# Kernel tuning notes

Hardware: AMD Instinct MI355X
Metric: run time of the kernel (lower is better)

## Reference

```python
import jax, jax.numpy as jnp
import numpy as np

BH, W, C, NHEAD = 512, 256, 128, 4
HEAD_DIM = C // NHEAD
EPS = 1e-5


def _xavier(key, shape):
    fan_out, fan_in = shape
    lim = np.sqrt(6.0 / (fan_in + fan_out)).astype(np.float32)
    return jax.random.uniform(key, shape, jnp.float32, -lim, lim)


def setup_inputs() -> dict:
    key = jax.random.key(0)
    ks = jax.random.split(key, 4)
    return {
        "feat_left": jax.random.normal(ks[0], (BH, W, C), jnp.float32),
        "feat_right": jax.random.normal(ks[1], (BH, W, C), jnp.float32),
        "l_proj_weight": _xavier(ks[2], (2 * C, C)),
        "r_proj_weight": _xavier(ks[3], (2 * C, C)),
        "l_proj_bias": jnp.zeros((2 * C,), jnp.float32),
        "r_proj_bias": jnp.zeros((2 * C,), jnp.float32),
        "l_out_weight": _xavier(jax.random.fold_in(key, 10), (C, C)),
        "l_out_bias": jnp.zeros((C,), jnp.float32),
        "r_out_weight": _xavier(jax.random.fold_in(key, 11), (C, C)),
        "r_out_bias": jnp.zeros((C,), jnp.float32),
        "norm_weight": jnp.ones((C,), jnp.float32),
        "norm_bias": jnp.zeros((C,), jnp.float32),
    }


def _layernorm(x, w, b):
    mu = jnp.mean(x, axis=-1, keepdims=True)
    var = jnp.mean(jnp.square(x - mu), axis=-1, keepdims=True)
    return (x - mu) * jax.lax.rsqrt(var + EPS) * w + b


def reference(feat_left, feat_right, l_proj_weight, r_proj_weight,
              l_proj_bias, r_proj_bias, l_out_weight, l_out_bias,
              r_out_weight, r_out_bias, norm_weight, norm_bias):
    bh, w, c = feat_left.shape
    e, hd = NHEAD, HEAD_DIM

    l_n = _layernorm(feat_left, norm_weight, norm_bias)
    r_n = _layernorm(feat_right, norm_weight, norm_bias)

    l_kv = l_n @ l_proj_weight.T + l_proj_bias
    r_kv = r_n @ r_proj_weight.T + r_proj_bias
    l_k, l_v = jnp.split(l_kv, 2, axis=-1)
    r_k, r_v = jnp.split(r_kv, 2, axis=-1)

    l_k = l_k.reshape(bh, w, e, hd)
    r_k = r_k.reshape(bh, w, e, hd)
    l_v = l_v.reshape(bh, w, e, hd)
    r_v = r_v.reshape(bh, w, e, hd)

    # shared score matrix [bh, heads, w_left, w_right]
    attn = jnp.einsum('nwec,nvec->newv', l_k, r_k) * 0.1

    # left attends over right positions (softmax over last axis)
    sm_l = jax.nn.softmax(attn, axis=-1)
    out_l = jnp.einsum('newv,nvec->nwec', sm_l, r_v).reshape(bh, w, c)

    # right attends over left positions (softmax over w axis of same scores)
    sm_r = jax.nn.softmax(attn, axis=2)
    out_r = jnp.einsum('newv,nwec->nvec', sm_r, l_v).reshape(bh, w, c)

    out_l = out_l @ l_out_weight.T + l_out_bias
    out_r = out_r @ r_out_weight.T + r_out_bias

    return feat_left + out_l, feat_right + out_r
```

## Files before the change

kernel.cpp:

```cpp
#include <hip/hip_runtime.h>
#include <hip/hip_bf16.h>

#define BH   512
#define NW   256
#define CC   128
#define TOK  (BH * NW)

typedef __attribute__((ext_vector_type(8))) short short8;
typedef __attribute__((ext_vector_type(4))) float f32x4;
typedef __attribute__((ext_vector_type(4))) int   i32x4;
typedef __attribute__((ext_vector_type(4))) unsigned short us4;
typedef __attribute__((ext_vector_type(2))) unsigned int u32x2;
typedef unsigned short ushort_t;

static __device__ __forceinline__ f32x4 mfma16(short8 a, short8 b, f32x4 c) {
    return __builtin_amdgcn_mfma_f32_16x16x32_bf16(a, b, c, 0, 0, 0);
}

static __device__ __forceinline__ unsigned int pk2(float a, float b) {
    __hip_bfloat162 h = __float22bfloat162_rn(make_float2(a, b));
    return *reinterpret_cast<unsigned int*>(&h);
}
static __device__ __forceinline__ ushort_t f2bf(float f) {
    unsigned int u = __float_as_uint(f);
    u = (u + 0x7fffu + ((u >> 16) & 1u)) >> 16;
    return (ushort_t)u;
}

__global__ __launch_bounds__(256)
void k_prep(const float* __restrict__ WpL, const float* __restrict__ WpR,
            const float* __restrict__ bpL, const float* __restrict__ bpR,
            const float* __restrict__ nw,  const float* __restrict__ nb,
            ushort_t* __restrict__ Wb, float* __restrict__ bias2)
{
    const int gid = blockIdx.x * 256 + threadIdx.x;
    const int row = gid >> 2;
    const int q   = gid & 3;
    const int side = row >> 8;
    const int o    = row & 255;
    const float* Wp = side ? WpR : WpL;
    const float* bp = side ? bpR : bpL;
    const float* wr = Wp + (size_t)o * 128 + q * 32;

    float acc = 0.f;
#pragma unroll
    for (int g = 0; g < 4; ++g) {
        const int c = q * 32 + g * 8;
        float4 wa = *(const float4*)(wr + g * 8);
        float4 wb = *(const float4*)(wr + g * 8 + 4);
        float4 ga = *(const float4*)(nw + c);
        float4 gb = *(const float4*)(nw + c + 4);
        float4 ba = *(const float4*)(nb + c);
        float4 bb = *(const float4*)(nb + c + 4);
        acc += wa.x*ba.x + wa.y*ba.y + wa.z*ba.z + wa.w*ba.w
             + wb.x*bb.x + wb.y*bb.y + wb.z*bb.z + wb.w*bb.w;
        u32x2 o0, o1;
        o0[0] = pk2(wa.x*ga.x, wa.y*ga.y);
        o0[1] = pk2(wa.z*ga.z, wa.w*ga.w);
        o1[0] = pk2(wb.x*gb.x, wb.y*gb.y);
        o1[1] = pk2(wb.z*gb.z, wb.w*gb.w);
        *(u32x2*)(Wb + (size_t)row * 128 + c)     = o0;
        *(u32x2*)(Wb + (size_t)row * 128 + c + 4) = o1;
    }
    acc += __shfl_xor(acc, 1);
    acc += __shfl_xor(acc, 2);
    if (q == 0) bias2[row] = bp[o] + acc;
}

__global__ __launch_bounds__(256)
void k_ln_proj(const float* __restrict__ featL, const float* __restrict__ featR,
               const ushort_t* __restrict__ Wb, const float* __restrict__ bias2,
               ushort_t* __restrict__ kvL,      ushort_t* __restrict__ kvR)
{
    const int side = blockIdx.y;
    const float* feat = side ? featR : featL;
    const ushort_t* W = Wb + side * 32768;
    const float* b2   = bias2 + side * 256;
    ushort_t*    kv   = side ? kvR : kvL;

    const int m0  = blockIdx.x * 64;
    const int tid = threadIdx.x;
    const int wid = tid >> 6, lane = tid & 63, l16 = lane & 15, lh = lane >> 4;
    const int wn  = wid * 64;

    __shared__ ushort_t smem[64 * 260];
    ushort_t (*Asm)[136] = (ushort_t (*)[136])smem;
    ushort_t (*kvS)[260] = (ushort_t (*)[260])smem;

    const int row = tid >> 2, q = tid & 3;
    const float* fr = feat + (size_t)(m0 + row) * CC + q * 32;
    float x[32];
#pragma unroll
    for (int i = 0; i < 8; ++i) {
        float4 v = *(const float4*)(fr + i * 4);
        x[i*4+0]=v.x; x[i*4+1]=v.y; x[i*4+2]=v.z; x[i*4+3]=v.w;
    }

    short8 Bf[16];
#pragma unroll
    for (int kk = 0; kk < 4; ++kk)
#pragma unroll
        for (int tn = 0; tn < 4; ++tn)
            Bf[kk*4 + tn] = *(const short8*)(W + (size_t)(wn + tn*16 + l16) * CC + kk*32 + lh*8);
    float4 bias[4];
#pragma unroll
    for (int tn = 0; tn < 4; ++tn)
        bias[tn] = *(const float4*)(b2 + wn + tn*16 + lh*4);

    {
        float s = 0.f, s2 = 0.f;
#pragma unroll
        for (int i = 0; i < 32; ++i) { s += x[i]; s2 += x[i]*x[i]; }
#pragma unroll
        for (int m = 1; m < 4; m <<= 1) { s += __shfl_xor(s, m); s2 += __shfl_xor(s2, m); }
        float mu   = s * (1.f / 128.f);
        float var  = s2 * (1.f / 128.f) - mu * mu;
        float rstd = rsqrtf(var + 1e-5f);
        float a = rstd, bsh = -mu * rstd;
#pragma unroll
        for (int g = 0; g < 4; ++g) {
            i32x4 o;
#pragma unroll
            for (int k = 0; k < 4; ++k)
                o[k] = (int)pk2(x[g*8 + 2*k] * a + bsh, x[g*8 + 2*k + 1] * a + bsh);
            *(i32x4*)&Asm[row][q * 32 + g * 8] = o;
        }
    }
    __syncthreads();

    f32x4 acc[4][4];
#pragma unroll
    for (int mt = 0; mt < 4; ++mt)
#pragma unroll
        for (int tn = 0; tn < 4; ++tn)
            acc[mt][tn] = (f32x4){0.f, 0.f, 0.f, 0.f};

#pragma unroll
    for (int kk = 0; kk < 4; ++kk) {
        short8 a[4];
#pragma unroll
        for (int mt = 0; mt < 4; ++mt)
            a[mt] = *(const short8*)&Asm[mt*16 + l16][kk*32 + lh*8];
#pragma unroll
        for (int tn = 0; tn < 4; ++tn)
#pragma unroll
            for (int mt = 0; mt < 4; ++mt)
                acc[mt][tn] = mfma16(Bf[kk*4 + tn], a[mt], acc[mt][tn]);
    }
    __syncthreads();

    const float kscale = (side == 0 && wn < 128) ? 0.14426950408889634f : 1.0f;
#pragma unroll
    for (int mt = 0; mt < 4; ++mt)
#pragma unroll
        for (int tn = 0; tn < 4; ++tn) {
            const int r    = mt*16 + l16;
            const int slot = (wn >> 2) + tn*4 + lh;
            float v0 = (acc[mt][tn][0] + bias[tn].x) * kscale;
            float v1 = (acc[mt][tn][1] + bias[tn].y) * kscale;
            float v2 = (acc[mt][tn][2] + bias[tn].z) * kscale;
            float v3 = (acc[mt][tn][3] + bias[tn].w) * kscale;
            u32x2 wv;
            wv[0] = pk2(v0, v1);
            wv[1] = pk2(v2, v3);
            *(u32x2*)&kvS[r][slot * 4] = wv;
        }
    __syncthreads();

#pragma unroll
    for (int it = 0; it < 16; ++it) {
        int u = it * 256 + tid;
        int r = u >> 6, sl = u & 63;
        u32x2 wv = *(const u32x2*)&kvS[r][sl * 4];
        *(u32x2*)(kv + (size_t)(m0 + r) * 256 + sl * 4) = wv;
    }
}

template<int BF16OUT>
__global__ __launch_bounds__(512, 4)
void k_attn(const ushort_t* __restrict__ kvL, const ushort_t* __restrict__ kvR,
            float* __restrict__ outFBase, ushort_t* __restrict__ outBBase)
{
    const int bx   = blockIdx.x;
    const int work = (bx & 7) * 512 + (bx >> 3);
    const int n    = work >> 3;
    const int e    = (work >> 1) & 3;
    const int dir  = work & 1;
    const ushort_t* kvA = dir ? kvR : kvL;
    const ushort_t* kvB = dir ? kvL : kvR;

    const int tid = threadIdx.x;
    const int wid = tid >> 6, lane = tid & 63, l16 = lane & 15, lh = lane >> 4;
    const int W0 = wid * 32;
    const int q  = l16 & 3;

    __shared__ ushort_t kB[256][32];
    __shared__ ushort_t vT[32][274];
    __shared__ ushort_t pL[8][32][32];

    {
        const ushort_t* src = kvB + (size_t)n * 256 * 256 + e * 32;
#pragma unroll
        for (int p = 0; p < 2; ++p) {
            int u = tid + p * 512;
            int r = u >> 2, slot = u & 3;
            *(i32x4*)&kB[r][(slot ^ (r & 3)) * 8] =
                *(const i32x4*)(src + (size_t)r * 256 + slot * 8);
        }
    }
    {
        const ushort_t* src = kvB + (size_t)n * 256 * 256 + 128 + e * 32;
#pragma unroll
        for (int u4 = 0; u4 < 4; ++u4) {
            int unit = tid + u4 * 512;
            int cp = unit & 15, vp = unit >> 4;
            unsigned int w0 = *(const unsigned int*)(src + (size_t)(vp*2    ) * 256 + cp*2);
            unsigned int w1 = *(const unsigned int*)(src + (size_t)(vp*2 + 1) * 256 + cp*2);
            *(unsigned int*)&vT[cp*2    ][vp*2] = (w0 & 0xffffu) | (w1 << 16);
            *(unsigned int*)&vT[cp*2 + 1][vp*2] = (w0 >> 16) | (w1 & 0xffff0000u);
        }
    }
    short8 aK[2];
#pragma unroll
    for (int tr = 0; tr < 2; ++tr)
        aK[tr] = *(const short8*)(kvA + (size_t)(n*256 + W0 + tr*16 + l16) * 256 + e*32 + lh*8);

    __syncthreads();

    f32x4 oacc[2][2];
#pragma unroll
    for (int tr = 0; tr < 2; ++tr)
#pragma unroll
        for (int ct = 0; ct < 2; ++ct)
            oacc[tr][ct] = (f32x4){0.f, 0.f, 0.f, 0.f};
    float lrun[2] = {0.f, 0.f};

#pragma unroll 2
    for (int nc = 0; nc < 8; ++nc) {
        const int vc0 = nc * 32;

        short8 bk0 = *(const short8*)&kB[vc0      + l16][8 * (lh ^ q)];
        short8 bk1 = *(const short8*)&kB[vc0 + 16 + l16][8 * (lh ^ q)];
        f32x4 s[2][2];
#pragma unroll
        for (int tr = 0; tr < 2; ++tr) {
            s[tr][0] = mfma16(bk0, aK[tr], (f32x4){0.f,0.f,0.f,0.f});
            s[tr][1] = mfma16(bk1, aK[tr], (f32x4){0.f,0.f,0.f,0.f});
        }

#pragma unroll
        for (int tr = 0; tr < 2; ++tr) {
#pragma unroll
            for (int tc = 0; tc < 2; ++tc) {
                float p0 = exp2f(s[tr][tc][0]);
                float p1 = exp2f(s[tr][tc][1]);
                float p2 = exp2f(s[tr][tc][2]);
                float p3 = exp2f(s[tr][tc][3]);
                lrun[tr] += (p0 + p1) + (p2 + p3);
                u32x2 w;
                w[0] = pk2(p0, p1);
                w[1] = pk2(p2, p3);
                *(u32x2*)&pL[wid][tr*16 + l16][(16*tc + 4*lh) ^ (8*q)] = w;
            }
        }

        short8 aP[2], bV[2];
#pragma unroll
        for (int tr = 0; tr < 2; ++tr)
            aP[tr] = *(const short8*)&pL[wid][tr*16 + l16][8 * (lh ^ q)];
#pragma unroll
        for (int ct = 0; ct < 2; ++ct)
            bV[ct] = *(const short8*)&vT[ct*16 + l16][vc0 + lh*8];
#pragma unroll
        for (int tr = 0; tr < 2; ++tr)
#pragma unroll
            for (int ct = 0; ct < 2; ++ct)
                oacc[tr][ct] = mfma16(bV[ct], aP[tr], oacc[tr][ct]);
    }

#pragma unroll
    for (int tr = 0; tr < 2; ++tr) {
        float sum = lrun[tr];
        sum += __shfl_xor(sum, 16);
        sum += __shfl_xor(sum, 32);
        float rinv = 1.f / sum;
        const int token = n * 256 + W0 + tr*16 + l16;
        if (BF16OUT) {
            ushort_t* outB = outBBase + (size_t)dir * TOK * CC;
#pragma unroll
            for (int ct = 0; ct < 2; ++ct) {
                us4 o;
#pragma unroll
                for (int j = 0; j < 4; ++j)
                    o[j] = f2bf(oacc[tr][ct][j] * rinv);
                *(us4*)(outB + (size_t)token * CC + e*32 + ct*16 + lh*4) = o;
            }
        } else {
            float* outF = outFBase + (size_t)dir * TOK * CC;
#pragma unroll
            for (int ct = 0; ct < 2; ++ct) {
                float4 o;
                o.x = oacc[tr][ct][0] * rinv;
                o.y = oacc[tr][ct][1] * rinv;
                o.z = oacc[tr][ct][2] * rinv;
                o.w = oacc[tr][ct][3] * rinv;
                *(float4*)(outF + (size_t)token * CC + e*32 + ct*16 + lh*4) = o;
            }
        }
    }
}

template<int BF16IN>
__global__ __launch_bounds__(512, 4)
void k_outproj(float* __restrict__ outBase, const ushort_t* __restrict__ aoutBase,
               const float* __restrict__ featL, const float* __restrict__ featR,
               const float* __restrict__ WoL,   const float* __restrict__ WoR,
               const float* __restrict__ boL,   const float* __restrict__ boR)
{
    const int side = blockIdx.y;
    float* io = outBase + (size_t)side * TOK * CC;
    const float* feat = side ? featR : featL;
    const float* Wo   = side ? WoR   : WoL;
    const float* bo   = side ? boR   : boL;

    const int m0 = blockIdx.x * 64;
    const int tid = threadIdx.x;

    __shared__ ushort_t Asm[64][136];
    __shared__ ushort_t Wsm[128][136];

#pragma unroll
    for (int i = 0; i < 8; ++i) {
        int u = tid + i * 512;
        int r = u >> 5, c4 = (u & 31) * 4;
        float4 w4 = *(const float4*)(Wo + (size_t)r * CC + c4);
        Wsm[r][c4+0] = f2bf(w4.x); Wsm[r][c4+1] = f2bf(w4.y);
        Wsm[r][c4+2] = f2bf(w4.z); Wsm[r][c4+3] = f2bf(w4.w);
    }
    if (BF16IN) {
        const ushort_t* src = aoutBase + (size_t)side * TOK * CC;
#pragma unroll
        for (int i = 0; i < 2; ++i) {
            int u = tid + i * 512;
            int r = u >> 4, c0 = (u & 15) * 8;
            *(i32x4*)&Asm[r][c0] = *(const i32x4*)(src + (size_t)(m0 + r) * CC + c0);
        }
    } else {
#pragma unroll
        for (int i = 0; i < 4; ++i) {
            int u = tid + i * 512;
            int r = u >> 5, c4 = (u & 31) * 4;
            float4 a4 = *(const float4*)(io + (size_t)(m0 + r) * CC + c4);
            Asm[r][c4+0] = f2bf(a4.x); Asm[r][c4+1] = f2bf(a4.y);
            Asm[r][c4+2] = f2bf(a4.z); Asm[r][c4+3] = f2bf(a4.w);
        }
    }
    __syncthreads();

    const int wid = tid >> 6, lane = tid & 63, l16 = lane & 15, lh = lane >> 4;
    const int wm = (wid >> 2) * 32;
    const int wn = (wid & 3) * 32;
    f32x4 acc[2][2];
#pragma unroll
    for (int tr = 0; tr < 2; ++tr)
#pragma unroll
        for (int nt = 0; nt < 2; ++nt)
            acc[tr][nt] = (f32x4){0.f, 0.f, 0.f, 0.f};

#pragma unroll
    for (int kk = 0; kk < 4; ++kk) {
        short8 a[2], b[2];
#pragma unroll
        for (int tr = 0; tr < 2; ++tr)
            a[tr] = *(const short8*)&Asm[wm + tr*16 + l16][kk*32 + lh*8];
#pragma unroll
        for (int nt = 0; nt < 2; ++nt)
            b[nt] = *(const short8*)&Wsm[wn + nt*16 + l16][kk*32 + lh*8];
#pragma unroll
        for (int tr = 0; tr < 2; ++tr)
#pragma unroll
            for (int nt = 0; nt < 2; ++nt)
                acc[tr][nt] = mfma16(a[tr], b[nt], acc[tr][nt]);
    }

#pragma unroll
    for (int tr = 0; tr < 2; ++tr)
#pragma unroll
        for (int nt = 0; nt < 2; ++nt) {
            int c = wn + nt*16 + l16;
            float bias = bo[c];
#pragma unroll
            for (int j = 0; j < 4; ++j) {
                int r = m0 + wm + tr*16 + lh*4 + j;
                io[(size_t)r * CC + c] = acc[tr][nt][j] + bias + feat[(size_t)r * CC + c];
            }
        }
}

extern "C" void kernel_launch(void* const* d_in, const int* in_sizes, int n_in,
                              void* d_out, int out_size, void* d_ws, size_t ws_size,
                              hipStream_t stream)
{
    const float* featL = (const float*)d_in[0];
    const float* featR = (const float*)d_in[1];
    const float* WpL   = (const float*)d_in[2];
    const float* WpR   = (const float*)d_in[3];
    const float* bpL   = (const float*)d_in[4];
    const float* bpR   = (const float*)d_in[5];
    const float* WoL   = (const float*)d_in[6];
    const float* boL   = (const float*)d_in[7];
    const float* WoR   = (const float*)d_in[8];
    const float* boR   = (const float*)d_in[9];
    const float* nw    = (const float*)d_in[10];
    const float* nb    = (const float*)d_in[11];

    float* out = (float*)d_out;
    ushort_t* kvL = (ushort_t*)d_ws;
    ushort_t* kvR = kvL + (size_t)TOK * 256;
    ushort_t* aout = kvR + (size_t)TOK * 256;
    ushort_t* Wb  = (ushort_t*)d_out;
    float* bias2  = (float*)d_out + 32768;

    const size_t need_bf16 = (size_t)TOK * 256 * 2 * 2 + (size_t)TOK * CC * 2 * 2;
    const bool bf16path = ws_size >= need_bf16;

    k_prep<<<dim3(8), 256, 0, stream>>>(WpL, WpR, bpL, bpR, nw, nb, Wb, bias2);
    k_ln_proj<<<dim3(2048, 2), 256, 0, stream>>>(featL, featR, Wb, bias2, kvL, kvR);
    if (bf16path) {
        k_attn<1><<<dim3(4096), 512, 0, stream>>>(kvL, kvR, out, aout);
        k_outproj<1><<<dim3(TOK / 64, 2), 512, 0, stream>>>(out, aout, featL, featR,
                                                            WoL, WoR, boL, boR);
    } else {
        k_attn<0><<<dim3(4096), 512, 0, stream>>>(kvL, kvR, out, aout);
        k_outproj<0><<<dim3(TOK / 64, 2), 512, 0, stream>>>(out, aout, featL, featR,
                                                            WoL, WoR, boL, boR);
    }
}
```

Baseline: 241.5 us.

## Rework LDS swizzles, use fast exp2, and compute softmax denominators via MFMA

Changes the XOR swizzle pattern for the K and P tiles in LDS to a pair-based class and pads the transposed V tile to a wider row stride, aiming to cut bank conflicts. Replaces exp2f with the hardware exp2 builtin. Computes the softmax row sums with an extra MFMA against a ones vector instead of scalar accumulation plus cross-lane shuffles. The denominator now sums the bf16-rounded probabilities, which matches the numerator's precision but adds MFMA work per chunk.

```diff
diff --git a/kernel.cpp b/kernel.cpp
--- a/kernel.cpp
+++ b/kernel.cpp
@@ -26,6 +26,11 @@
     u = (u + 0x7fffu + ((u >> 16) & 1u)) >> 16;
     return (ushort_t)u;
 }
+#if __has_builtin(__builtin_amdgcn_exp2f)
+static __device__ __forceinline__ float exp2_fast(float x) { return __builtin_amdgcn_exp2f(x); }
+#else
+static __device__ __forceinline__ float exp2_fast(float x) { return exp2f(x); }
+#endif
 
 __global__ __launch_bounds__(256)
 void k_prep(const float* __restrict__ WpL, const float* __restrict__ WpR,
@@ -192,10 +197,10 @@
     const int tid = threadIdx.x;
     const int wid = tid >> 6, lane = tid & 63, l16 = lane & 15, lh = lane >> 4;
     const int W0 = wid * 32;
-    const int q  = l16 & 3;
+    const int kcls = (l16 >> 1) & 3;
 
     __shared__ ushort_t kB[256][32];
-    __shared__ ushort_t vT[32][274];
+    __shared__ ushort_t vT[32][280];
     __shared__ ushort_t pL[8][32][32];
 
     {
@@ -204,7 +209,7 @@
         for (int p = 0; p < 2; ++p) {
             int u = tid + p * 512;
             int r = u >> 2, slot = u & 3;
-            *(i32x4*)&kB[r][(slot ^ (r & 3)) * 8] =
+            *(i32x4*)&kB[r][(slot ^ ((r >> 1) & 3)) << 3] =
                 *(const i32x4*)(src + (size_t)r * 256 + slot * 8);
         }
     }
@@ -225,6 +230,10 @@
     for (int tr = 0; tr < 2; ++tr)
         aK[tr] = *(const short8*)(kvA + (size_t)(n*256 + W0 + tr*16 + l16) * 256 + e*32 + lh*8);
 
+    short8 ones;
+#pragma unroll
+    for (int i = 0; i < 8; ++i) ones[i] = (short)0x3F80;
+
     __syncthreads();
 
     f32x4 oacc[2][2];
@@ -233,14 +242,14 @@
 #pragma unroll
         for (int ct = 0; ct < 2; ++ct)
             oacc[tr][ct] = (f32x4){0.f, 0.f, 0.f, 0.f};
-    float lrun[2] = {0.f, 0.f};
+    f32x4 lacc[2] = {(f32x4){0.f,0.f,0.f,0.f}, (f32x4){0.f,0.f,0.f,0.f}};
 
 #pragma unroll 2
     for (int nc = 0; nc < 8; ++nc) {
         const int vc0 = nc * 32;
 
-        short8 bk0 = *(const short8*)&kB[vc0      + l16][8 * (lh ^ q)];
-        short8 bk1 = *(const short8*)&kB[vc0 + 16 + l16][8 * (lh ^ q)];
+        short8 bk0 = *(const short8*)&kB[vc0      + l16][(lh ^ kcls) << 3];
+        short8 bk1 = *(const short8*)&kB[vc0 + 16 + l16][(lh ^ kcls) << 3];
         f32x4 s[2][2];
 #pragma unroll
         for (int tr = 0; tr < 2; ++tr) {
@@ -250,40 +259,41 @@
 
 #pragma unroll
         for (int tr = 0; tr < 2; ++tr) {
+            const int prow = tr*16 + l16;
 #pragma unroll
             for (int tc = 0; tc < 2; ++tc) {
-                float p0 = exp2f(s[tr][tc][0]);
-                float p1 = exp2f(s[tr][tc][1]);
-                float p2 = exp2f(s[tr][tc][2]);
-                float p3 = exp2f(s[tr][tc][3]);
-                lrun[tr] += (p0 + p1) + (p2 + p3);
+                float p0 = exp2_fast(s[tr][tc][0]);
+                float p1 = exp2_fast(s[tr][tc][1]);
+                float p2 = exp2_fast(s[tr][tc][2]);
+                float p3 = exp2_fast(s[tr][tc][3]);
                 u32x2 w;
                 w[0] = pk2(p0, p1);
                 w[1] = pk2(p2, p3);
-                *(u32x2*)&pL[wid][tr*16 + l16][(16*tc + 4*lh) ^ (8*q)] = w;
+                const int sL   = 2*tc + (lh >> 1);
+                const int pcol = ((sL ^ kcls) << 3) + ((lh & 1) << 2);
+                *(u32x2*)&pL[wid][prow][pcol] = w;
             }
         }
 
         short8 aP[2], bV[2];
 #pragma unroll
         for (int tr = 0; tr < 2; ++tr)
-            aP[tr] = *(const short8*)&pL[wid][tr*16 + l16][8 * (lh ^ q)];
+            aP[tr] = *(const short8*)&pL[wid][tr*16 + l16][(lh ^ kcls) << 3];
 #pragma unroll
         for (int ct = 0; ct < 2; ++ct)
             bV[ct] = *(const short8*)&vT[ct*16 + l16][vc0 + lh*8];
 #pragma unroll
-        for (int tr = 0; tr < 2; ++tr)
+        for (int tr = 0; tr < 2; ++tr) {
 #pragma unroll
             for (int ct = 0; ct < 2; ++ct)
                 oacc[tr][ct] = mfma16(bV[ct], aP[tr], oacc[tr][ct]);
+            lacc[tr] = mfma16(ones, aP[tr], lacc[tr]);
+        }
     }
 
 #pragma unroll
     for (int tr = 0; tr < 2; ++tr) {
-        float sum = lrun[tr];
-        sum += __shfl_xor(sum, 16);
-        sum += __shfl_xor(sum, 32);
-        float rinv = 1.f / sum;
+        float rinv = 1.f / lacc[tr][0];
         const int token = n * 256 + W0 + tr*16 + l16;
         if (BF16OUT) {
             ushort_t* outB = outBBase + (size_t)dir * TOK * CC;
```

New measurement: 214.2 us. 1.13x faster.
